# Kernel tuning notes

Hardware: AMD Instinct MI355X
Metric: run time of the kernel (lower is better)

The kernel has to match this reference:

```python
import jax, jax.numpy as jnp
import numpy as np

IN_F = 1024   # in_features
OUT_F = 1024  # out_features
N = 32768     # flattened batch (prod of x.shape[:-1]))
K = 3         # clones per rewire -> denom = K + 1


def setup_inputs() -> dict:
    key = jax.random.key(0)
    k1, k2, k3, k4 = jax.random.split(key, 4)
    bound = 1.0 / np.sqrt(IN_F)
    x = jax.random.normal(k1, (N, IN_F), dtype=jnp.float32)
    # kaiming-uniform-ish init scale for weight, uniform(-bound,bound) for bias
    weight = jax.random.uniform(k2, (OUT_F, IN_F), dtype=jnp.float32,
                                minval=-bound, maxval=bound) * np.sqrt(3.0)
    bias = jax.random.uniform(k3, (OUT_F,), dtype=jnp.float32,
                              minval=-bound, maxval=bound)
    # one rewire per output row; clones are distinct from src (dead-neuron slots)
    rewire_rows = jnp.arange(OUT_F, dtype=jnp.int32)
    rewire_src = jax.random.randint(k4, (OUT_F,), 0, IN_F, dtype=jnp.int32)
    rewire_clones = (rewire_src[:, None] + jnp.arange(1, K + 1, dtype=jnp.int32)) % IN_F
    return {"x": x, "weight": weight, "bias": bias,
            "rewire_rows": rewire_rows, "rewire_src": rewire_src,
            "rewire_clones": rewire_clones}


def reference(x, weight, bias, rewire_rows, rewire_src, rewire_clones):
    # Plain linear part, shared by all output rows: y = x @ W^T + b
    base = x @ weight.T + bias                                  # [N, OUT_F]

    # Per-rewire correction. For rewire e on row r with src s and clones d_k
    # (denom = K+1), the torch loop replaces x[:, s] -> x[:, s]/denom and
    # x[:, d_k] -> x[:, s]/denom before the GEMV with weight[r].
    # Equivalent delta added to base[:, r] (indices within a rewire are disjoint):
    denom = rewire_clones.shape[1] + 1                          # K + 1
    xs = x[:, rewire_src]                                       # [N, R]
    new_val = xs / denom                                        # [N, R]
    w_src = weight[rewire_rows, rewire_src]                     # [R]
    delta = (new_val - xs) * w_src                              # src column change
    xc = x[:, rewire_clones]                                    # [N, R, K]
    wc = weight[rewire_rows[:, None], rewire_clones]            # [R, K]
    delta = delta + jnp.einsum('nrk,rk->nr', new_val[:, :, None] - xc, wc)

    # Scatter-add the deltas into their output rows (duplicates accumulate).
    return base.at[:, rewire_rows].add(delta)                   # [N, OUT_F]
```

## Files before the change

### kernel.cpp

```cpp
#include <hip/hip_runtime.h>

#define IN_F 1024
#define OUT_F 1024
#define NTOK 32768
#define BM 128
#define BN 128
#define BK 32
#define KT (IN_F / BK)

typedef __bf16 bf16;
typedef __bf16 bf16x4 __attribute__((ext_vector_type(4)));
typedef __bf16 bf16x8 __attribute__((ext_vector_type(8)));
typedef float f32x4 __attribute__((ext_vector_type(4)));

__global__ void build_wp(const float* __restrict__ W,
                         const int* __restrict__ rows,
                         const int* __restrict__ srcs,
                         const int* __restrict__ clones,
                         bf16* __restrict__ Wp) {
  const int r = blockIdx.x;
  const int row = rows[r];
  const int s = srcs[r];
  const int c0 = clones[3 * r + 0];
  const int c1 = clones[3 * r + 1];
  const int c2 = clones[3 * r + 2];
  const float* wr = W + (size_t)row * IN_F;
  const float fixv = 0.25f * (wr[s] + wr[c0] + wr[c1] + wr[c2]);

  const int col = threadIdx.x * 4;
  f32x4 v = *reinterpret_cast<const f32x4*>(wr + col);
  bf16x4 o;
#pragma unroll
  for (int j = 0; j < 4; ++j) {
    const int c = col + j;
    float f = v[j];
    if (c == c0 || c == c1 || c == c2) f = 0.0f;
    if (c == s) f = fixv;
    o[j] = (bf16)f;
  }
  *reinterpret_cast<bf16x4*>(Wp + (size_t)row * IN_F + col) = o;
}

__device__ __forceinline__ void load_a(const float* __restrict__ gA, int kt,
                                       f32x4* dst) {
#pragma unroll
  for (int j = 0; j < 4; ++j)
    dst[j] = *reinterpret_cast<const f32x4*>(gA + (size_t)(j * 32) * IN_F +
                                             kt * BK);
}

__global__ __launch_bounds__(256, 3) void gemm_rewire(
    const float* __restrict__ X, const bf16* __restrict__ Wp,
    const float* __restrict__ bias, float* __restrict__ out) {
  __shared__ __align__(16) bf16 lA[BM * BK];
  __shared__ __align__(16) bf16 lB[BN * BK];

  const int tid = threadIdx.x;
  const int lane = tid & 63;
  const int w = tid >> 6;
  const int wr = w >> 1;
  const int wc = w & 1;
  const int bm = blockIdx.x;
  const int bn = blockIdx.y;

  const int ar = tid >> 3;
  const int ac = (tid & 7) * 4;
  const float* gA = X + ((size_t)bm * BM + ar) * IN_F + ac;

  const int brow = w * 16 + (lane >> 2);
  const int bcol = (lane & 3) * 8;
  const bf16* gB = Wp + ((size_t)bn * BN + brow) * IN_F + bcol;
  bf16* lB_base = lB + w * 512;

  f32x4 acc[4][4];
#pragma unroll
  for (int n = 0; n < 4; ++n) {
    const float bv = bias[bn * BN + wc * 64 + n * 16 + (lane & 15)];
#pragma unroll
    for (int m = 0; m < 4; ++m) acc[m][n] = (f32x4){bv, bv, bv, bv};
  }

  const int afoff = (wr * 64 + (lane & 15)) * BK + (lane >> 4) * 8;
  const int bfoff = (wc * 64 + (lane & 15)) * BK + (lane >> 4) * 8;

  f32x4 av[4];
  load_a(gA, 0, av);

  for (int kt = 0; kt < KT; ++kt) {
    if (kt > 0) __syncthreads();

#pragma unroll
    for (int j = 0; j < 4; ++j) {
      bf16x4 o;
      o[0] = (bf16)av[j][0];
      o[1] = (bf16)av[j][1];
      o[2] = (bf16)av[j][2];
      o[3] = (bf16)av[j][3];
      *reinterpret_cast<bf16x4*>(lA + (j * 32 + ar) * BK + ac) = o;
    }

    const bf16* gBk = gB + kt * BK;
    __builtin_amdgcn_global_load_lds(
        (const __attribute__((address_space(1))) void*)gBk,
        (__attribute__((address_space(3))) void*)lB_base, 16, 0, 0);
    __builtin_amdgcn_global_load_lds(
        (const __attribute__((address_space(1))) void*)(gBk + (size_t)64 * IN_F),
        (__attribute__((address_space(3))) void*)(lB_base + 2048), 16, 0, 0);

    __syncthreads();

    const bool pf = (kt + 1) < KT;
    f32x4 avn[4];
    if (pf) load_a(gA, kt + 1, avn);

    bf16x8 af[4], bfr[4];
#pragma unroll
    for (int m = 0; m < 4; ++m)
      af[m] = *reinterpret_cast<const bf16x8*>(lA + afoff + m * 16 * BK);
#pragma unroll
    for (int n = 0; n < 4; ++n)
      bfr[n] = *reinterpret_cast<const bf16x8*>(lB + bfoff + n * 16 * BK);

#pragma unroll
    for (int m = 0; m < 4; ++m)
#pragma unroll
      for (int n = 0; n < 4; ++n)
        acc[m][n] = __builtin_amdgcn_mfma_f32_16x16x32_bf16(af[m], bfr[n],
                                                            acc[m][n], 0, 0, 0);

    if (pf) {
#pragma unroll
      for (int j = 0; j < 4; ++j) av[j] = avn[j];
    }
  }

  const int orow0 = bm * BM + wr * 64 + (lane >> 4) * 4;
  const int ocol0 = bn * BN + wc * 64 + (lane & 15);
#pragma unroll
  for (int m = 0; m < 4; ++m) {
#pragma unroll
    for (int n = 0; n < 4; ++n) {
      const f32x4 v = acc[m][n];
      const size_t base = (size_t)(orow0 + m * 16) * OUT_F + (ocol0 + n * 16);
#pragma unroll
      for (int i = 0; i < 4; ++i) out[base + (size_t)i * OUT_F] = v[i];
    }
  }
}

extern "C" void kernel_launch(void* const* d_in, const int* in_sizes, int n_in,
                              void* d_out, int out_size, void* d_ws,
                              size_t ws_size, hipStream_t stream) {
  const float* x = (const float*)d_in[0];
  const float* weight = (const float*)d_in[1];
  const float* bias = (const float*)d_in[2];
  const int* rrows = (const int*)d_in[3];
  const int* rsrc = (const int*)d_in[4];
  const int* rclones = (const int*)d_in[5];
  float* out = (float*)d_out;
  bf16* Wp = (bf16*)d_ws;

  build_wp<<<dim3(OUT_F), dim3(256), 0, stream>>>(weight, rrows, rsrc, rclones,
                                                  Wp);
  gemm_rewire<<<dim3(NTOK / BM, OUT_F / BN), dim3(256), 0, stream>>>(x, Wp,
                                                                     bias, out);
}
```

Baseline: 127.2 us.

## Double-buffer LDS with swizzled layout and deeper K tile in GEMM

Doubles the K tile from 32 to 64 and adds two LDS buffers, so global loads for step t+2 and LDS writes for step t+1 overlap the MFMA work on step t. Waits are done with hand-placed s_waitcnt and s_barrier. LDS rows use an XOR swizzle on both the A and B tiles to avoid bank conflicts at the wider row stride. The kernel now launches with 2 blocks per CU instead of 3, because LDS and register use go up; this costs occupancy, and the manual vmcnt accounting is fragile.

```diff
diff --git a/kernel.cpp b/kernel.cpp
--- a/kernel.cpp
+++ b/kernel.cpp
@@ -5,7 +5,7 @@
 #define NTOK 32768
 #define BM 128
 #define BN 128
-#define BK 32
+#define BK 64
 #define KT (IN_F / BK)
 
 typedef __bf16 bf16;
@@ -41,19 +41,11 @@
   *reinterpret_cast<bf16x4*>(Wp + (size_t)row * IN_F + col) = o;
 }
 
-__device__ __forceinline__ void load_a(const float* __restrict__ gA, int kt,
-                                       f32x4* dst) {
-#pragma unroll
-  for (int j = 0; j < 4; ++j)
-    dst[j] = *reinterpret_cast<const f32x4*>(gA + (size_t)(j * 32) * IN_F +
-                                             kt * BK);
-}
-
-__global__ __launch_bounds__(256, 3) void gemm_rewire(
+__global__ __launch_bounds__(256, 2) void gemm_rewire(
     const float* __restrict__ X, const bf16* __restrict__ Wp,
     const float* __restrict__ bias, float* __restrict__ out) {
-  __shared__ __align__(16) bf16 lA[BM * BK];
-  __shared__ __align__(16) bf16 lB[BN * BK];
+  __shared__ __align__(16) bf16 lA[2][BM * BK];
+  __shared__ __align__(16) bf16 lB[2][BN * BK];
 
   const int tid = threadIdx.x;
   const int lane = tid & 63;
@@ -63,14 +55,14 @@
   const int bm = blockIdx.x;
   const int bn = blockIdx.y;
 
-  const int ar = tid >> 3;
-  const int ac = (tid & 7) * 4;
-  const float* gA = X + ((size_t)bm * BM + ar) * IN_F + ac;
+  const float* gA =
+      X + ((size_t)bm * BM + (tid >> 4)) * IN_F + (tid & 15) * 4;
+  const int arx7 = (tid >> 4) & 7;
+  const int awbyte0 =
+      (tid >> 4) * 128 + (((((tid & 15) >> 1)) ^ arx7) * 16) + (tid & 1) * 8;
 
-  const int brow = w * 16 + (lane >> 2);
-  const int bcol = (lane & 3) * 8;
-  const bf16* gB = Wp + ((size_t)bn * BN + brow) * IN_F + bcol;
-  bf16* lB_base = lB + w * 512;
+  const bf16* gB = Wp + ((size_t)bn * BN + w * 8 + (lane >> 3)) * IN_F +
+                   (((lane & 7) ^ (lane >> 3)) * 8);
 
   f32x4 acc[4][4];
 #pragma unroll
@@ -80,57 +72,93 @@
     for (int m = 0; m < 4; ++m) acc[m][n] = (f32x4){bv, bv, bv, bv};
   }
 
-  const int afoff = (wr * 64 + (lane & 15)) * BK + (lane >> 4) * 8;
-  const int bfoff = (wc * 64 + (lane & 15)) * BK + (lane >> 4) * 8;
+  const int arow = wr * 64 + (lane & 15);
+  const int brow = wc * 64 + (lane & 15);
+  const int slot0 = lane >> 4;
+  const int ax7 = arow & 7;
+  const int bx7 = brow & 7;
 
-  f32x4 av[4];
-  load_a(gA, 0, av);
+  f32x4 av[8];
 
-  for (int kt = 0; kt < KT; ++kt) {
-    if (kt > 0) __syncthreads();
-
+  auto issueA = [&](int kt2) {
 #pragma unroll
-    for (int j = 0; j < 4; ++j) {
+    for (int j = 0; j < 8; ++j)
+      av[j] = *reinterpret_cast<const f32x4*>(gA + (size_t)j * 16 * IN_F +
+                                              (size_t)kt2 * BK);
+  };
+  auto writeA = [&](int buf) {
+    char* base = (char*)lA[buf];
+#pragma unroll
+    for (int j = 0; j < 8; ++j) {
       bf16x4 o;
       o[0] = (bf16)av[j][0];
       o[1] = (bf16)av[j][1];
       o[2] = (bf16)av[j][2];
       o[3] = (bf16)av[j][3];
-      *reinterpret_cast<bf16x4*>(lA + (j * 32 + ar) * BK + ac) = o;
+      *reinterpret_cast<bf16x4*>(base + j * 2048 + awbyte0) = o;
     }
-
-    const bf16* gBk = gB + kt * BK;
-    __builtin_amdgcn_global_load_lds(
-        (const __attribute__((address_space(1))) void*)gBk,
-        (__attribute__((address_space(3))) void*)lB_base, 16, 0, 0);
-    __builtin_amdgcn_global_load_lds(
-        (const __attribute__((address_space(1))) void*)(gBk + (size_t)64 * IN_F),
-        (__attribute__((address_space(3))) void*)(lB_base + 2048), 16, 0, 0);
-
-    __syncthreads();
-
-    const bool pf = (kt + 1) < KT;
-    f32x4 avn[4];
-    if (pf) load_a(gA, kt + 1, avn);
-
-    bf16x8 af[4], bfr[4];
+  };
+  auto issueB = [&](int kt2, int buf) {
+    const bf16* g = gB + (size_t)kt2 * BK;
 #pragma unroll
-    for (int m = 0; m < 4; ++m)
-      af[m] = *reinterpret_cast<const bf16x8*>(lA + afoff + m * 16 * BK);
+    for (int i = 0; i < 4; ++i) {
+      char* dst = (char*)lB[buf] + i * 4096 + w * 1024;
+      __builtin_amdgcn_global_load_lds(
+          (const __attribute__((address_space(1))) void*)(g +
+                                                          (size_t)i * 32 * IN_F),
+          (__attribute__((address_space(3))) void*)dst, 16, 0, 0);
+    }
+  };
+  auto compute = [&](int buf) {
+    const char* A = (const char*)lA[buf];
+    const char* B = (const char*)lB[buf];
 #pragma unroll
-    for (int n = 0; n < 4; ++n)
-      bfr[n] = *reinterpret_cast<const bf16x8*>(lB + bfoff + n * 16 * BK);
-
+    for (int kk = 0; kk < 2; ++kk) {
+      const int sa = ((slot0 + kk * 4) ^ ax7) * 16;
+      const int sb = ((slot0 + kk * 4) ^ bx7) * 16;
+      bf16x8 af[4], bfr[4];
 #pragma unroll
-    for (int m = 0; m < 4; ++m)
+      for (int m = 0; m < 4; ++m)
+        af[m] = *reinterpret_cast<const bf16x8*>(A + (arow + m * 16) * 128 + sa);
 #pragma unroll
       for (int n = 0; n < 4; ++n)
-        acc[m][n] = __builtin_amdgcn_mfma_f32_16x16x32_bf16(af[m], bfr[n],
-                                                            acc[m][n], 0, 0, 0);
+        bfr[n] =
+            *reinterpret_cast<const bf16x8*>(B + (brow + n * 16) * 128 + sb);
+#pragma unroll
+      for (int m = 0; m < 4; ++m)
+#pragma unroll
+        for (int n = 0; n < 4; ++n)
+          acc[m][n] = __builtin_amdgcn_mfma_f32_16x16x32_bf16(
+              af[m], bfr[n], acc[m][n], 0, 0, 0);
+    }
+  };
 
-    if (pf) {
-#pragma unroll
-      for (int j = 0; j < 4; ++j) av[j] = avn[j];
+  issueA(0);
+  issueB(0, 0);
+  __builtin_amdgcn_sched_barrier(0);
+  writeA(0);
+  issueA(1);
+  asm volatile("s_waitcnt vmcnt(8) lgkmcnt(0)" ::: "memory");
+  __builtin_amdgcn_s_barrier();
+  issueB(1, 1);
+  __builtin_amdgcn_sched_barrier(0);
+
+  int cur = 0;
+  for (int t = 0; t < KT; ++t) {
+    if (t + 1 < KT) writeA(cur ^ 1);
+    if (t + 2 < KT) issueA(t + 2);
+    compute(cur);
+    if (t + 1 < KT) {
+      if (t + 2 < KT)
+        asm volatile("s_waitcnt vmcnt(8) lgkmcnt(0)" ::: "memory");
+      else
+        asm volatile("s_waitcnt vmcnt(0) lgkmcnt(0)" ::: "memory");
+      __builtin_amdgcn_s_barrier();
+      if (t + 2 < KT) {
+        issueB(t + 2, cur);
+        __builtin_amdgcn_sched_barrier(0);
+      }
+      cur ^= 1;
     }
   }
 
```

Measured after the change: 150.9 us. 1.19x slower.

## Load A fragments directly from global and double-buffer swizzled B tiles in LDS

Applied to the files above, without the earlier changes.

Changes the GEMM tiling to 64x256 tiles with BK=64 on a 1D grid whose block order groups neighbouring row tiles. The A (activation) operand is no longer staged in LDS: each wave loads its fp32 fragments straight from global memory and converts them to bf16 in registers. The B (weight) tile is double-buffered in LDS with an XOR swizzle, and the next tile is prefetched asynchronously while MFMAs run. This removes the LDS write/read of A and one barrier per step. In exchange, every wave reloads the same A rows redundantly from global/L2, register pressure rises, and launch bounds drop to two blocks per SM.

```diff
diff --git a/kernel.cpp b/kernel.cpp
--- a/kernel.cpp
+++ b/kernel.cpp
@@ -3,9 +3,9 @@
 #define IN_F 1024
 #define OUT_F 1024
 #define NTOK 32768
-#define BM 128
-#define BN 128
-#define BK 32
+#define BMT 64
+#define BNT 256
+#define BK 64
 #define KT (IN_F / BK)
 
 typedef __bf16 bf16;
@@ -41,107 +41,101 @@
   *reinterpret_cast<bf16x4*>(Wp + (size_t)row * IN_F + col) = o;
 }
 
-__device__ __forceinline__ void load_a(const float* __restrict__ gA, int kt,
-                                       f32x4* dst) {
-#pragma unroll
-  for (int j = 0; j < 4; ++j)
-    dst[j] = *reinterpret_cast<const f32x4*>(gA + (size_t)(j * 32) * IN_F +
-                                             kt * BK);
-}
-
-__global__ __launch_bounds__(256, 3) void gemm_rewire(
+__global__ __launch_bounds__(256, 2) void gemm_rewire(
     const float* __restrict__ X, const bf16* __restrict__ Wp,
     const float* __restrict__ bias, float* __restrict__ out) {
-  __shared__ __align__(16) bf16 lA[BM * BK];
-  __shared__ __align__(16) bf16 lB[BN * BK];
+  __shared__ __align__(16) bf16 lB[2][BNT * BK];
 
   const int tid = threadIdx.x;
   const int lane = tid & 63;
   const int w = tid >> 6;
-  const int wr = w >> 1;
-  const int wc = w & 1;
-  const int bm = blockIdx.x;
-  const int bn = blockIdx.y;
 
-  const int ar = tid >> 3;
-  const int ac = (tid & 7) * 4;
-  const float* gA = X + ((size_t)bm * BM + ar) * IN_F + ac;
+  const int bid = blockIdx.x;
+  const int seq = bid >> 3;
+  const int bm = (bid & 7) + 8 * (seq >> 2);
+  const int bn = seq & 3;
 
-  const int brow = w * 16 + (lane >> 2);
-  const int bcol = (lane & 3) * 8;
-  const bf16* gB = Wp + ((size_t)bn * BN + brow) * IN_F + bcol;
-  bf16* lB_base = lB + w * 512;
+  const float* gA =
+      X + ((size_t)bm * BMT + (lane & 15)) * IN_F + (lane >> 4) * 8;
+
+  const bf16* gB = Wp + ((size_t)bn * BNT + w * 8 + (lane >> 3)) * IN_F +
+                   (((lane & 7) ^ ((lane >> 3) & 7)) * 8);
 
   f32x4 acc[4][4];
 #pragma unroll
   for (int n = 0; n < 4; ++n) {
-    const float bv = bias[bn * BN + wc * 64 + n * 16 + (lane & 15)];
+    const float bv = bias[bn * BNT + w * 64 + n * 16 + (lane & 15)];
 #pragma unroll
     for (int m = 0; m < 4; ++m) acc[m][n] = (f32x4){bv, bv, bv, bv};
   }
 
-  const int afoff = (wr * 64 + (lane & 15)) * BK + (lane >> 4) * 8;
-  const int bfoff = (wc * 64 + (lane & 15)) * BK + (lane >> 4) * 8;
+  const int bcol0 = w * 64 + (lane & 15);
+  const int lx7 = lane & 7;
+  const int sl0 = lane >> 4;
 
-  f32x4 av[4];
-  load_a(gA, 0, av);
+  auto issueB = [&](int t, int buf) {
+    const bf16* g = gB + t * BK;
+#pragma unroll
+    for (int i = 0; i < 8; ++i) {
+      char* dst = (char*)lB[buf] + i * 4096 + w * 1024;
+      __builtin_amdgcn_global_load_lds(
+          (const __attribute__((address_space(1))) void*)(g +
+                                                          (size_t)i * 32 * IN_F),
+          (__attribute__((address_space(3))) void*)dst, 16, 0, 0);
+    }
+  };
 
-  for (int kt = 0; kt < KT; ++kt) {
-    if (kt > 0) __syncthreads();
+  issueB(0, 0);
+  __syncthreads();
 
 #pragma unroll
-    for (int j = 0; j < 4; ++j) {
-      bf16x4 o;
-      o[0] = (bf16)av[j][0];
-      o[1] = (bf16)av[j][1];
-      o[2] = (bf16)av[j][2];
-      o[3] = (bf16)av[j][3];
-      *reinterpret_cast<bf16x4*>(lA + (j * 32 + ar) * BK + ac) = o;
-    }
-
-    const bf16* gBk = gB + kt * BK;
-    __builtin_amdgcn_global_load_lds(
-        (const __attribute__((address_space(1))) void*)gBk,
-        (__attribute__((address_space(3))) void*)lB_base, 16, 0, 0);
-    __builtin_amdgcn_global_load_lds(
-        (const __attribute__((address_space(1))) void*)(gBk + (size_t)64 * IN_F),
-        (__attribute__((address_space(3))) void*)(lB_base + 2048), 16, 0, 0);
-
-    __syncthreads();
-
-    const bool pf = (kt + 1) < KT;
-    f32x4 avn[4];
-    if (pf) load_a(gA, kt + 1, avn);
-
-    bf16x8 af[4], bfr[4];
-#pragma unroll
-    for (int m = 0; m < 4; ++m)
-      af[m] = *reinterpret_cast<const bf16x8*>(lA + afoff + m * 16 * BK);
-#pragma unroll
-    for (int n = 0; n < 4; ++n)
-      bfr[n] = *reinterpret_cast<const bf16x8*>(lB + bfoff + n * 16 * BK);
-
+  for (int t = 0; t < KT; ++t) {
+    f32x4 av[4][2][2];
 #pragma unroll
     for (int m = 0; m < 4; ++m)
 #pragma unroll
-      for (int n = 0; n < 4; ++n)
-        acc[m][n] = __builtin_amdgcn_mfma_f32_16x16x32_bf16(af[m], bfr[n],
-                                                            acc[m][n], 0, 0, 0);
+      for (int kk = 0; kk < 2; ++kk) {
+        const float* p = gA + (size_t)m * 16 * IN_F + t * BK + kk * 32;
+        av[m][kk][0] = *reinterpret_cast<const f32x4*>(p);
+        av[m][kk][1] = *reinterpret_cast<const f32x4*>(p + 4);
+      }
+    if (t + 1 < KT) issueB(t + 1, (t + 1) & 1);
 
-    if (pf) {
+    const char* B = (const char*)lB[t & 1];
 #pragma unroll
-      for (int j = 0; j < 4; ++j) av[j] = avn[j];
+    for (int kk = 0; kk < 2; ++kk) {
+      bf16x8 bfr[4];
+#pragma unroll
+      for (int n = 0; n < 4; ++n) {
+        const int col = bcol0 + n * 16;
+        bfr[n] = *reinterpret_cast<const bf16x8*>(
+            B + col * 128 + (((kk * 4 + sl0) ^ lx7) * 16));
+      }
+#pragma unroll
+      for (int m = 0; m < 4; ++m) {
+        bf16x8 af;
+#pragma unroll
+        for (int q = 0; q < 4; ++q) {
+          af[q] = (bf16)av[m][kk][0][q];
+          af[4 + q] = (bf16)av[m][kk][1][q];
+        }
+#pragma unroll
+        for (int n = 0; n < 4; ++n)
+          acc[m][n] = __builtin_amdgcn_mfma_f32_16x16x32_bf16(af, bfr[n],
+                                                              acc[m][n], 0, 0, 0);
+      }
     }
+    __syncthreads();
   }
 
-  const int orow0 = bm * BM + wr * 64 + (lane >> 4) * 4;
-  const int ocol0 = bn * BN + wc * 64 + (lane & 15);
+  const int orow0 = bm * BMT + (lane >> 4) * 4;
+  const int ocol = bn * BNT + w * 64 + (lane & 15);
 #pragma unroll
   for (int m = 0; m < 4; ++m) {
 #pragma unroll
     for (int n = 0; n < 4; ++n) {
       const f32x4 v = acc[m][n];
-      const size_t base = (size_t)(orow0 + m * 16) * OUT_F + (ocol0 + n * 16);
+      const size_t base = (size_t)(orow0 + m * 16) * OUT_F + (ocol + n * 16);
 #pragma unroll
       for (int i = 0; i < 4; ++i) out[base + (size_t)i * OUT_F] = v[i];
     }
@@ -162,6 +156,6 @@
 
   build_wp<<<dim3(OUT_F), dim3(256), 0, stream>>>(weight, rrows, rsrc, rclones,
                                                   Wp);
-  gemm_rewire<<<dim3(NTOK / BM, OUT_F / BN), dim3(256), 0, stream>>>(x, Wp,
-                                                                     bias, out);
+  gemm_rewire<<<dim3((NTOK / BMT) * (OUT_F / BNT)), dim3(256), 0, stream>>>(
+      x, Wp, bias, out);
 }
```

Result: slower. 288.8 us (+127.0%).
